# Optimization experiments

Measured on AMD Instinct MI355X. Metric: run time of the kernel, lower is better.

The kernel has to match this reference:

```python
import jax, jax.numpy as jnp
import numpy as np

B, T, C = 16, 512, 768
MULT = 4
D_IN = C * MULT          # 3072
HIDDEN = 1024
N_DATES = 16
STACK_SIZE, STACK_STRIDE = 4, 2
MAX_F = 512
N_MASK_TYPES = 5
N_SESSIONS = 4
SCALE = HIDDEN ** 0.5


def setup_inputs() -> dict:
    key = jax.random.key(0)
    ks = jax.random.split(key, 12)
    inp = {
        "spikes": jax.random.normal(ks[0], (B, T, C), dtype=jnp.float32),
        "spikes_mask": jnp.ones((B, T), dtype=jnp.int64),
        "spikes_timestamp": jax.random.randint(ks[1], (B, T), 0, 255).astype(jnp.int64),
        "date_idx": jax.random.randint(ks[2], (B,), 0, N_DATES).astype(jnp.int64),
        "mask_idx": 1,
        "session_idx": 3,
        # params
        "W_embed": jax.random.normal(ks[3], (N_DATES, D_IN, C), dtype=jnp.float32) * 0.02,
        "b_embed": jax.random.normal(ks[4], (N_DATES, D_IN), dtype=jnp.float32) * 0.02,
        "W_stack": jax.random.normal(ks[5], (HIDDEN, D_IN * STACK_SIZE), dtype=jnp.float32) * 0.02,
        "b_stack": jax.random.normal(ks[6], (HIDDEN,), dtype=jnp.float32) * 0.02,
        "pos_table": jax.random.normal(ks[7], (MAX_F, HIDDEN), dtype=jnp.float32) * 0.02,
        "prompt_table": jax.random.normal(ks[8], (N_MASK_TYPES, HIDDEN), dtype=jnp.float32) * 0.02,
        "session_table": jax.random.normal(ks[9], (N_SESSIONS, HIDDEN), dtype=jnp.float32) * 0.02,
    }
    return inp


def reference(spikes, spikes_mask, spikes_timestamp, date_idx, mask_idx, session_idx,
              W_embed, b_embed, W_stack, b_stack, pos_table, prompt_table, session_table):
    Bb = spikes.shape[0]
    # adapt branch: per-sample expert Linear, done as one gather + batched GEMM
    W = W_embed[date_idx]                      # [B, D_IN, C]
    b = b_embed[date_idx]                      # [B, D_IN]
    x = jnp.einsum('btc,bdc->btd', spikes, W) + b[:, None, :]   # [B, T, D_IN]
    x = jax.nn.gelu(x, approximate=False) * SCALE
    # unfold-based stacking: sliding windows over time
    L = (T - STACK_SIZE) // STACK_STRIDE + 1   # 255
    starts = jnp.arange(L) * STACK_STRIDE
    widx = starts[:, None] + jnp.arange(STACK_SIZE)             # [L, size]
    win = x[:, widx, :]                                         # [B, L, size, D_IN]
    stacked = win.reshape(Bb, L, STACK_SIZE * D_IN)
    x = stacked @ W_stack.T + b_stack                           # [B, L, HIDDEN]
    ts = spikes_timestamp[:, :L]
    mask = jnp.prod(spikes_mask[:, widx], axis=-1)              # [B, L]
    # positional embedding
    x = x + pos_table[ts]
    # prompt token
    x = jnp.concatenate(
        [jnp.broadcast_to(prompt_table[mask_idx][None, None, :], (Bb, 1, HIDDEN)), x], axis=1)
    mask = jnp.pad(mask, ((0, 0), (1, 0)), constant_values=1)
    ts = jnp.concatenate([jnp.zeros((Bb, 1), ts.dtype), ts + 1], axis=1)
    # session token
    x = jnp.concatenate(
        [jnp.broadcast_to(session_table[session_idx][None, None, :], (Bb, 1, HIDDEN)), x], axis=1)
    mask = jnp.pad(mask, ((0, 0), (1, 0)), constant_values=1)
    ts = jnp.concatenate([jnp.zeros((Bb, 1), ts.dtype), ts + 1], axis=1)
    # dropout is identity in eval
    return x, mask, ts
```

## Files before the change

kernel.cpp:

```cpp
#include <hip/hip_runtime.h>
#include <hip/hip_bf16.h>

#define BATCH   16
#define TT      512
#define CC      768
#define D_IN    3072
#define HIDDEN  1024
#define LL      255
#define OUTROWS 257
#define KSTACK  12288
#define N_DATES 16

typedef float f32x4 __attribute__((ext_vector_type(4)));
typedef __bf16 bf16x8 __attribute__((ext_vector_type(8)));
typedef unsigned short u16;

__device__ __forceinline__ u16 f2bf(float f) {
    unsigned u = __builtin_bit_cast(unsigned, f);
    u = (u + 0x7FFFu + ((u >> 16) & 1u)) >> 16;
    return (u16)u;
}

__device__ __forceinline__ bf16x8 lds_read8(const u16* p) {
    return __builtin_bit_cast(bf16x8, *(const uint4*)p);
}

__device__ __forceinline__ void gload16(const u16* g, u16* l) {
    __builtin_amdgcn_global_load_lds(
        (const __attribute__((address_space(1))) void*)g,
        (__attribute__((address_space(3))) void*)l, 16, 0, 0);
}

__global__ __launch_bounds__(256) void cvt_wstack(const float* __restrict__ W, u16* __restrict__ out) {
    size_t i = ((size_t)blockIdx.x * 256 + threadIdx.x) * 4;
    size_t stride = (size_t)gridDim.x * 256 * 4;
    for (; i < (size_t)HIDDEN * KSTACK; i += stride) {
        float4 v = *(const float4*)(W + i);
        ushort4 o = make_ushort4(f2bf(v.x), f2bf(v.y), f2bf(v.z), f2bf(v.w));
        *(ushort4*)(out + i) = o;
    }
}

__global__ __launch_bounds__(256) void cvt_spikes(const float* __restrict__ in, u16* __restrict__ out) {
    size_t i = ((size_t)blockIdx.x * 256 + threadIdx.x) * 4;
    size_t stride = (size_t)gridDim.x * 256 * 4;
    for (; i < (size_t)BATCH * TT * CC; i += stride) {
        float4 v = *(const float4*)(in + i);
        ushort4 o = make_ushort4(f2bf(v.x), f2bf(v.y), f2bf(v.z), f2bf(v.w));
        *(ushort4*)(out + i) = o;
    }
}

__global__ __launch_bounds__(64) void date_flags(const int* __restrict__ date_idx, int* __restrict__ flags) {
    const int tid = threadIdx.x;
    if (tid < N_DATES) flags[tid] = 0;
    __syncthreads();
    if (tid < BATCH) flags[date_idx[tid]] = 1;
}

__global__ __launch_bounds__(256) void cvt_wembed(const float* __restrict__ W,
                                                  const int* __restrict__ flags,
                                                  u16* __restrict__ out) {
    const int date = blockIdx.y;
    if (!flags[date]) return;
    const size_t bofs = (size_t)date * D_IN * CC;
    const size_t i = bofs + ((size_t)blockIdx.x * 256 + threadIdx.x) * 4;
    float4 v = *(const float4*)(W + i);
    ushort4 o = make_ushort4(f2bf(v.x), f2bf(v.y), f2bf(v.z), f2bf(v.w));
    *(ushort4*)(out + i) = o;
}

__global__ __launch_bounds__(512, 2) void gemm1_bf(const u16* __restrict__ spk,
                                                   const u16* __restrict__ wemb,
                                                   const float* __restrict__ b_embed,
                                                   const int* __restrict__ date_idx,
                                                   u16* __restrict__ x1) {
    const int m0 = blockIdx.x * 256;
    const int n0 = blockIdx.y * 256;
    const int bb = blockIdx.z;
    const int date = date_idx[bb];
    const u16* A  = spk  + (size_t)bb   * TT * CC;
    const u16* Bw = wemb + (size_t)date * D_IN * CC;
    const int nt = CC / 64;

    __shared__ u16 Asm[2 * 256 * 64];
    __shared__ u16 Bsm[2 * 256 * 64];

    const int tid  = threadIdx.x;
    const int lane = tid & 63;
    const int wave = tid >> 6;
    const int wm = wave >> 2;
    const int wn = wave & 3;

    const int lrow = lane >> 3;
    const int scol = ((lane & 7) ^ lrow) << 3;

    f32x4 acc[8][4] = {};

    auto STAGE = [&](int k0, int buf) {
        u16* Ad = Asm + buf * (256 * 64);
        u16* Bd = Bsm + buf * (256 * 64);
        #pragma unroll
        for (int i = 0; i < 4; ++i) {
            const int rb = i * 8 + wave;
            const int row = rb * 8 + lrow;
            gload16(A  + (size_t)(m0 + row) * CC + k0 + scol, Ad + rb * 512);
            gload16(Bw + (size_t)(n0 + row) * CC + k0 + scol, Bd + rb * 512);
        }
    };

    STAGE(0, 0);
    STAGE(64, 1);

    for (int t = 0; t < nt; ++t) {
        const int cur = t & 1;
        if (t + 1 < nt) { asm volatile("s_waitcnt vmcnt(8)" ::: "memory"); }
        else            { asm volatile("s_waitcnt vmcnt(0)" ::: "memory"); }
        __builtin_amdgcn_s_barrier();
        asm volatile("" ::: "memory");

        const u16* Ab = Asm + cur * (256 * 64);
        const u16* Bb = Bsm + cur * (256 * 64);
        #pragma unroll
        for (int kk = 0; kk < 64; kk += 32) {
            bf16x8 af[8], bfr[4];
            const int krow = lane & 15;
            const int kcol = kk + ((lane >> 4) << 3);
            #pragma unroll
            for (int i = 0; i < 8; ++i) {
                const int ra = wm * 128 + i * 16 + krow;
                af[i] = lds_read8(&Ab[ra * 64 + (kcol ^ ((ra & 7) << 3))]);
            }
            #pragma unroll
            for (int j = 0; j < 4; ++j) {
                const int rb2 = wn * 64 + j * 16 + krow;
                bfr[j] = lds_read8(&Bb[rb2 * 64 + (kcol ^ ((rb2 & 7) << 3))]);
            }
            #pragma unroll
            for (int i = 0; i < 8; ++i)
                #pragma unroll
                for (int j = 0; j < 4; ++j)
                    acc[i][j] = __builtin_amdgcn_mfma_f32_16x16x32_bf16(af[i], bfr[j], acc[i][j], 0, 0, 0);
        }

        asm volatile("" ::: "memory");
        __builtin_amdgcn_s_barrier();
        asm volatile("" ::: "memory");
        if (t + 2 < nt) STAGE((t + 2) * 64, cur);
    }

    const float* be = b_embed + (size_t)date * D_IN;
    #pragma unroll
    for (int i = 0; i < 8; ++i) {
        #pragma unroll
        for (int j = 0; j < 4; ++j) {
            const int col  = n0 + wn * 64 + j * 16 + (lane & 15);
            const float bias = be[col];
            const int rbase = m0 + wm * 128 + i * 16 + ((lane >> 4) << 2);
            #pragma unroll
            for (int q = 0; q < 4; ++q) {
                float v = acc[i][j][q] + bias;
                float g = 0.5f * v * (1.0f + erff(v * 0.70710678118654752f)) * 32.0f;
                x1[(size_t)bb * TT * D_IN + (size_t)(rbase + q) * D_IN + col] = f2bf(g);
            }
        }
    }
}

__global__ __launch_bounds__(256) void gemm1_f32(const float* __restrict__ spikes,
                                                 const float* __restrict__ W_embed,
                                                 const float* __restrict__ b_embed,
                                                 const int* __restrict__ date_idx,
                                                 u16* __restrict__ x1) {
    const int m0 = blockIdx.x * 128;
    const int n0 = blockIdx.y * 128;
    const int bb = blockIdx.z;
    const int date = date_idx[bb];
    const float* A  = spikes  + (size_t)bb  * TT * CC;
    const float* Bw = W_embed + (size_t)date * D_IN * CC;

    __shared__ u16 As[128 * 64];
    __shared__ u16 Bs[128 * 64];

    const int tid  = threadIdx.x;
    const int lane = tid & 63;
    const int wave = tid >> 6;
    const int wm = wave >> 1, wn = wave & 1;

    f32x4 acc[4][4] = {};

    for (int k0 = 0; k0 < CC; k0 += 64) {
        {
            const int c4 = tid & 15;
            int r = tid >> 4;
            #pragma unroll
            for (int p = 0; p < 8; ++p, r += 16) {
                float4 va = *(const float4*)(A  + (size_t)(m0 + r) * CC + k0 + c4 * 4);
                float4 vb = *(const float4*)(Bw + (size_t)(n0 + r) * CC + k0 + c4 * 4);
                const int col = c4 * 4;
                const int idx = r * 64 + (col ^ ((r & 7) << 3));
                *(ushort4*)(&As[idx]) = make_ushort4(f2bf(va.x), f2bf(va.y), f2bf(va.z), f2bf(va.w));
                *(ushort4*)(&Bs[idx]) = make_ushort4(f2bf(vb.x), f2bf(vb.y), f2bf(vb.z), f2bf(vb.w));
            }
        }
        __syncthreads();
        #pragma unroll
        for (int kk = 0; kk < 64; kk += 32) {
            bf16x8 af[4], bfr[4];
            const int krow = lane & 15;
            const int kcol = kk + ((lane >> 4) << 3);
            #pragma unroll
            for (int i = 0; i < 4; ++i) {
                const int ra = wm * 64 + i * 16 + krow;
                af[i]  = lds_read8(&As[ra * 64 + (kcol ^ ((ra & 7) << 3))]);
                const int rb = wn * 64 + i * 16 + krow;
                bfr[i] = lds_read8(&Bs[rb * 64 + (kcol ^ ((rb & 7) << 3))]);
            }
            #pragma unroll
            for (int i = 0; i < 4; ++i)
                #pragma unroll
                for (int j = 0; j < 4; ++j)
                    acc[i][j] = __builtin_amdgcn_mfma_f32_16x16x32_bf16(af[i], bfr[j], acc[i][j], 0, 0, 0);
        }
        __syncthreads();
    }

    const float* be = b_embed + (size_t)date * D_IN;
    #pragma unroll
    for (int i = 0; i < 4; ++i) {
        #pragma unroll
        for (int j = 0; j < 4; ++j) {
            const int col  = n0 + wn * 64 + j * 16 + (lane & 15);
            const float bias = be[col];
            const int rbase = m0 + wm * 64 + i * 16 + ((lane >> 4) << 2);
            #pragma unroll
            for (int q = 0; q < 4; ++q) {
                float v = acc[i][j][q] + bias;
                float g = 0.5f * v * (1.0f + erff(v * 0.70710678118654752f)) * 32.0f;
                x1[(size_t)bb * TT * D_IN + (size_t)(rbase + q) * D_IN + col] = f2bf(g);
            }
        }
    }
}

template <bool WRITE_PART>
__global__ __launch_bounds__(512, 2) void gemm2(const u16* __restrict__ x1,
                                                const u16* __restrict__ Wbf,
                                                float* __restrict__ part,
                                                const float* __restrict__ b_stack,
                                                const float* __restrict__ pos_table,
                                                const int* __restrict__ tstamp,
                                                float* __restrict__ out,
                                                int KS) {
    const int n0 = blockIdx.x * 256;
    const int ks = blockIdx.y;
    const int bb = blockIdx.z;
    const int KCH  = KSTACK / KS;
    const int kbeg = ks * KCH;
    const int nt   = KCH / 64;
    const u16* Xb = x1 + (size_t)bb * TT * D_IN;

    __shared__ u16 Asm[2 * 256 * 64];
    __shared__ u16 Bsm[2 * 256 * 64];

    const int tid  = threadIdx.x;
    const int lane = tid & 63;
    const int wave = tid >> 6;
    const int wm = wave >> 2;
    const int wn = wave & 3;

    const int lrow = lane >> 3;
    const int scol = ((lane & 7) ^ lrow) << 3;

    f32x4 acc[8][4] = {};

    auto STAGE = [&](int k0, int buf) {
        const int s  = k0 / D_IN;
        const int d0 = k0 % D_IN;
        u16* Ad = Asm + buf * (256 * 64);
        u16* Bd = Bsm + buf * (256 * 64);
        #pragma unroll
        for (int i = 0; i < 4; ++i) {
            const int rb = i * 8 + wave;
            const int row = rb * 8 + lrow;
            int gl = row; if (gl > LL - 1) gl = LL - 1;
            gload16(Xb + (size_t)(2 * gl + s) * D_IN + d0 + scol, Ad + rb * 512);
            gload16(Wbf + (size_t)(n0 + row) * KSTACK + k0 + scol, Bd + rb * 512);
        }
    };

    STAGE(kbeg, 0);
    STAGE(kbeg + 64, 1);

    for (int t = 0; t < nt; ++t) {
        const int cur = t & 1;
        if (t + 1 < nt) { asm volatile("s_waitcnt vmcnt(8)" ::: "memory"); }
        else            { asm volatile("s_waitcnt vmcnt(0)" ::: "memory"); }
        __builtin_amdgcn_s_barrier();
        asm volatile("" ::: "memory");

        const u16* Ab = Asm + cur * (256 * 64);
        const u16* Bb = Bsm + cur * (256 * 64);
        #pragma unroll
        for (int kk = 0; kk < 64; kk += 32) {
            bf16x8 af[8], bfr[4];
            const int krow = lane & 15;
            const int kcol = kk + ((lane >> 4) << 3);
            #pragma unroll
            for (int i = 0; i < 8; ++i) {
                const int ra = wm * 128 + i * 16 + krow;
                af[i] = lds_read8(&Ab[ra * 64 + (kcol ^ ((ra & 7) << 3))]);
            }
            #pragma unroll
            for (int j = 0; j < 4; ++j) {
                const int rb2 = wn * 64 + j * 16 + krow;
                bfr[j] = lds_read8(&Bb[rb2 * 64 + (kcol ^ ((rb2 & 7) << 3))]);
            }
            #pragma unroll
            for (int i = 0; i < 8; ++i)
                #pragma unroll
                for (int j = 0; j < 4; ++j)
                    acc[i][j] = __builtin_amdgcn_mfma_f32_16x16x32_bf16(af[i], bfr[j], acc[i][j], 0, 0, 0);
        }

        asm volatile("" ::: "memory");
        __builtin_amdgcn_s_barrier();
        asm volatile("" ::: "memory");
        if (t + 2 < nt) STAGE(kbeg + (t + 2) * 64, cur);
    }

    if (WRITE_PART) {
        float* pt = part + ((size_t)(ks * BATCH + bb) * 256) * HIDDEN;
        #pragma unroll
        for (int i = 0; i < 8; ++i) {
            #pragma unroll
            for (int j = 0; j < 4; ++j) {
                const int col = n0 + wn * 64 + j * 16 + (lane & 15);
                const int rb  = wm * 128 + i * 16 + ((lane >> 4) << 2);
                #pragma unroll
                for (int q = 0; q < 4; ++q)
                    pt[(size_t)(rb + q) * HIDDEN + col] = acc[i][j][q];
            }
        }
    } else {
        #pragma unroll
        for (int i = 0; i < 8; ++i) {
            #pragma unroll
            for (int j = 0; j < 4; ++j) {
                const int col = n0 + wn * 64 + j * 16 + (lane & 15);
                const int lb  = wm * 128 + i * 16 + ((lane >> 4) << 2);
                #pragma unroll
                for (int q = 0; q < 4; ++q) {
                    const int l = lb + q;
                    if (l < LL) {
                        const int tsv = tstamp[bb * TT + l];
                        float v = acc[i][j][q] + b_stack[col] + pos_table[(size_t)tsv * HIDDEN + col];
                        out[(size_t)bb * OUTROWS * HIDDEN + (size_t)(2 + l) * HIDDEN + col] = v;
                    }
                }
            }
        }
    }
}

__global__ __launch_bounds__(256) void reduce_ep(const float* __restrict__ part,
                                                 const float* __restrict__ b_stack,
                                                 const float* __restrict__ pos_table,
                                                 const int* __restrict__ tstamp,
                                                 float* __restrict__ out,
                                                 int KS) {
    const int idx = blockIdx.x * 256 + threadIdx.x;
    const int c4  = idx & (HIDDEN / 4 - 1);
    const int r   = idx >> 8;
    if (r >= BATCH * LL) return;
    const int l  = r % LL;
    const int bb = r / LL;
    float4 v = make_float4(0.f, 0.f, 0.f, 0.f);
    for (int ks = 0; ks < KS; ++ks) {
        float4 p = *(const float4*)(part + ((size_t)(ks * BATCH + bb) * 256 + l) * HIDDEN + c4 * 4);
        v.x += p.x; v.y += p.y; v.z += p.z; v.w += p.w;
    }
    const int tsv = tstamp[bb * TT + l];
    float4 bs = *(const float4*)(b_stack + c4 * 4);
    float4 ps = *(const float4*)(pos_table + (size_t)tsv * HIDDEN + c4 * 4);
    v.x += bs.x + ps.x; v.y += bs.y + ps.y; v.z += bs.z + ps.z; v.w += bs.w + ps.w;
    *(float4*)(out + ((size_t)bb * OUTROWS + 2 + l) * HIDDEN + c4 * 4) = v;
}

__global__ __launch_bounds__(256) void epilogue_misc(const int* __restrict__ smask,
                                                     const int* __restrict__ tstamp,
                                                     const int* __restrict__ mask_idx_p,
                                                     const int* __restrict__ session_idx_p,
                                                     const float* __restrict__ prompt_table,
                                                     const float* __restrict__ session_table,
                                                     float* __restrict__ out) {
    const int bb = blockIdx.x;
    const int tid = threadIdx.x;
    const int mi = mask_idx_p[0];
    const int si = session_idx_p[0];
    float* xb = out + (size_t)bb * OUTROWS * HIDDEN;
    for (int i = tid; i < HIDDEN; i += 256) {
        xb[i]          = session_table[(size_t)si * HIDDEN + i];
        xb[HIDDEN + i] = prompt_table[(size_t)mi * HIDDEN + i];
    }
    float* maskout = out + (size_t)BATCH * OUTROWS * HIDDEN + (size_t)bb * OUTROWS;
    float* tsout   = out + (size_t)BATCH * OUTROWS * HIDDEN + (size_t)BATCH * OUTROWS + (size_t)bb * OUTROWS;
    for (int j = tid; j < OUTROWS; j += 256) {
        if (j == 0)      { maskout[0] = 1.0f; tsout[0] = 0.0f; }
        else if (j == 1) { maskout[1] = 1.0f; tsout[1] = 1.0f; }
        else {
            const int l = j - 2;
            int m = 1;
            #pragma unroll
            for (int s = 0; s < 4; ++s) m *= smask[bb * TT + 2 * l + s];
            maskout[j] = (float)m;
            tsout[j]   = (float)(tstamp[bb * TT + l] + 2);
        }
    }
}

extern "C" void kernel_launch(void* const* d_in, const int* in_sizes, int n_in,
                              void* d_out, int out_size, void* d_ws, size_t ws_size,
                              hipStream_t stream) {
    const float* spikes      = (const float*)d_in[0];
    const int*   spikes_mask = (const int*)d_in[1];
    const int*   tstamp      = (const int*)d_in[2];
    const int*   date_idx    = (const int*)d_in[3];
    const int*   mask_idx    = (const int*)d_in[4];
    const int*   session_idx = (const int*)d_in[5];
    const float* W_embed     = (const float*)d_in[6];
    const float* b_embed     = (const float*)d_in[7];
    const float* W_stack     = (const float*)d_in[8];
    const float* b_stack     = (const float*)d_in[9];
    const float* pos_table   = (const float*)d_in[10];
    const float* prompt_tab  = (const float*)d_in[11];
    const float* session_tab = (const float*)d_in[12];
    float* out = (float*)d_out;

    const size_t X1_B   = (size_t)BATCH * TT * D_IN * 2;
    const size_t WBF_B  = (size_t)HIDDEN * KSTACK * 2;
    const size_t PART_B = (size_t)BATCH * 256 * HIDDEN * 4;
    const size_t FLAGS_B = 4096;
    const size_t SPK_B  = (size_t)BATCH * TT * CC * 2;
    const size_t WEMB_B = (size_t)N_DATES * D_IN * CC * 2;
    const size_t BASE   = X1_B + WBF_B;
    const size_t UNION_BF = FLAGS_B + SPK_B + WEMB_B;

    u16*   x1    = (u16*)d_ws;
    u16*   Wbf   = (u16*)((char*)d_ws + X1_B);
    int*   flags = (int*)((char*)d_ws + BASE);
    u16*   spkbf = (u16*)((char*)d_ws + BASE + FLAGS_B);
    u16*   wembf = (u16*)((char*)d_ws + BASE + FLAGS_B + SPK_B);
    float* part  = (float*)((char*)d_ws + BASE);

    const bool use_bf = (ws_size >= BASE + UNION_BF);
    int KS = 0;
    if (use_bf) KS = 4;
    else {
        size_t rem = (ws_size > BASE) ? (ws_size - BASE) : 0;
        KS = (int)(rem / PART_B); if (KS > 4) KS = 4;
    }

    cvt_wstack<<<2048, 256, 0, stream>>>(W_stack, Wbf);

    if (use_bf) {
        date_flags<<<1, 64, 0, stream>>>(date_idx, flags);
        cvt_spikes<<<2048, 256, 0, stream>>>(spikes, spkbf);
        cvt_wembed<<<dim3(D_IN * CC / 4 / 256, N_DATES), 256, 0, stream>>>(W_embed, flags, wembf);
        gemm1_bf<<<dim3(TT / 256, D_IN / 256, BATCH), 512, 0, stream>>>(spkbf, wembf, b_embed, date_idx, x1);
    } else {
        gemm1_f32<<<dim3(TT / 128, D_IN / 128, BATCH), 256, 0, stream>>>(spikes, W_embed, b_embed, date_idx, x1);
    }

    if (KS > 0) {
        gemm2<true><<<dim3(HIDDEN / 256, KS, BATCH), 512, 0, stream>>>(x1, Wbf, part, b_stack, pos_table, tstamp, out, KS);
        reduce_ep<<<(BATCH * LL * (HIDDEN / 4) + 255) / 256, 256, 0, stream>>>(part, b_stack, pos_table, tstamp, out, KS);
    } else {
        gemm2<false><<<dim3(HIDDEN / 256, 1, BATCH), 512, 0, stream>>>(x1, Wbf, part, b_stack, pos_table, tstamp, out, 1);
    }
    epilogue_misc<<<BATCH, 256, 0, stream>>>(spikes_mask, tstamp, mask_idx, session_idx,
                                             prompt_tab, session_tab, out);
}
```

Baseline: 265.0 us.

## Use 4-slot 32-wide K pipeline with one barrier per step in gemm2

Restructures the stacking GEMM's main loop from a double-buffered 64-wide K tile with two barriers per iteration into a 4-slot ring of 32-wide K slices, three slices in flight, and a single barrier per step. The LDS layout packs two rows' half-tiles per 64-element line. The next slice is issued right after fragments are read, and the MFMA block is wrapped in s_setprio to favour math issue. This aims to hide global-load latency and cut barrier stalls, at the cost of more complex swizzle indexing and finer-grained waitcnt bookkeeping that must match the load count.

```diff
diff --git a/kernel.cpp b/kernel.cpp
--- a/kernel.cpp
+++ b/kernel.cpp
@@ -257,11 +257,11 @@
     const int bb = blockIdx.z;
     const int KCH  = KSTACK / KS;
     const int kbeg = ks * KCH;
-    const int nt   = KCH / 64;
+    const int S    = KCH / 32;
     const u16* Xb = x1 + (size_t)bb * TT * D_IN;
 
-    __shared__ u16 Asm[2 * 256 * 64];
-    __shared__ u16 Bsm[2 * 256 * 64];
+    __shared__ u16 Asm[4][128 * 64];
+    __shared__ u16 Bsm[4][128 * 64];
 
     const int tid  = threadIdx.x;
     const int lane = tid & 63;
@@ -269,64 +269,64 @@
     const int wm = wave >> 2;
     const int wn = wave & 3;
 
-    const int lrow = lane >> 3;
-    const int scol = ((lane & 7) ^ lrow) << 3;
+    const int lrow  = lane >> 3;
+    const int scol  = ((lane & 7) ^ lrow) << 3;
+    const int chalf = scol >> 5;
+    const int gk    = scol & 31;
 
     f32x4 acc[8][4] = {};
 
-    auto STAGE = [&](int k0, int buf) {
+    auto STAGE = [&](int slice) {
+        const int slot = slice & 3;
+        const int k0 = kbeg + slice * 32;
         const int s  = k0 / D_IN;
         const int d0 = k0 % D_IN;
-        u16* Ad = Asm + buf * (256 * 64);
-        u16* Bd = Bsm + buf * (256 * 64);
-        #pragma unroll
-        for (int i = 0; i < 4; ++i) {
-            const int rb = i * 8 + wave;
-            const int row = rb * 8 + lrow;
-            int gl = row; if (gl > LL - 1) gl = LL - 1;
-            gload16(Xb + (size_t)(2 * gl + s) * D_IN + d0 + scol, Ad + rb * 512);
-            gload16(Wbf + (size_t)(n0 + row) * KSTACK + k0 + scol, Bd + rb * 512);
+        u16* Ad = Asm[slot];
+        u16* Bd = Bsm[slot];
+        #pragma unroll
+        for (int p = 0; p < 2; ++p) {
+            const int rbase = (wave + 8 * p) * 8;
+            const int u  = rbase + lrow;
+            const int tr = 2 * u + chalf;
+            int gl = tr; if (gl > LL - 1) gl = LL - 1;
+            gload16(Xb + (size_t)(2 * gl + s) * D_IN + d0 + gk, Ad + rbase * 64);
+            gload16(Wbf + (size_t)(n0 + tr) * KSTACK + k0 + gk, Bd + rbase * 64);
         }
     };
 
-    STAGE(kbeg, 0);
-    STAGE(kbeg + 64, 1);
-
-    for (int t = 0; t < nt; ++t) {
-        const int cur = t & 1;
-        if (t + 1 < nt) { asm volatile("s_waitcnt vmcnt(8)" ::: "memory"); }
-        else            { asm volatile("s_waitcnt vmcnt(0)" ::: "memory"); }
+    STAGE(0); STAGE(1); STAGE(2);
+
+    const int krow  = lane & 15;
+    const int kcol  = (lane >> 4) << 3;
+    const int cfrag = (kcol + ((krow & 1) << 5)) ^ ((krow >> 1) << 3);
+    const int urow  = krow >> 1;
+
+    for (int ph = 0; ph < S; ++ph) {
+        if (ph < S - 2)       { asm volatile("s_waitcnt vmcnt(8)" ::: "memory"); }
+        else if (ph == S - 2) { asm volatile("s_waitcnt vmcnt(4)" ::: "memory"); }
+        else                  { asm volatile("s_waitcnt vmcnt(0)" ::: "memory"); }
         __builtin_amdgcn_s_barrier();
         asm volatile("" ::: "memory");
 
-        const u16* Ab = Asm + cur * (256 * 64);
-        const u16* Bb = Bsm + cur * (256 * 64);
-        #pragma unroll
-        for (int kk = 0; kk < 64; kk += 32) {
-            bf16x8 af[8], bfr[4];
-            const int krow = lane & 15;
-            const int kcol = kk + ((lane >> 4) << 3);
-            #pragma unroll
-            for (int i = 0; i < 8; ++i) {
-                const int ra = wm * 128 + i * 16 + krow;
-                af[i] = lds_read8(&Ab[ra * 64 + (kcol ^ ((ra & 7) << 3))]);
-            }
-            #pragma unroll
-            for (int j = 0; j < 4; ++j) {
-                const int rb2 = wn * 64 + j * 16 + krow;
-                bfr[j] = lds_read8(&Bb[rb2 * 64 + (kcol ^ ((rb2 & 7) << 3))]);
-            }
-            #pragma unroll
-            for (int i = 0; i < 8; ++i)
-                #pragma unroll
-                for (int j = 0; j < 4; ++j)
-                    acc[i][j] = __builtin_amdgcn_mfma_f32_16x16x32_bf16(af[i], bfr[j], acc[i][j], 0, 0, 0);
-        }
-
-        asm volatile("" ::: "memory");
-        __builtin_amdgcn_s_barrier();
-        asm volatile("" ::: "memory");
-        if (t + 2 < nt) STAGE(kbeg + (t + 2) * 64, cur);
+        const u16* Ab = Asm[ph & 3];
+        const u16* Bb = Bsm[ph & 3];
+        bf16x8 af[8], bfr[4];
+        #pragma unroll
+        for (int i = 0; i < 8; ++i)
+            af[i] = lds_read8(&Ab[(wm * 64 + i * 8 + urow) * 64 + cfrag]);
+        #pragma unroll
+        for (int j = 0; j < 4; ++j)
+            bfr[j] = lds_read8(&Bb[(wn * 32 + j * 8 + urow) * 64 + cfrag]);
+
+        if (ph + 3 < S) STAGE(ph + 3);
+
+        __builtin_amdgcn_s_setprio(1);
+        #pragma unroll
+        for (int i = 0; i < 8; ++i)
+            #pragma unroll
+            for (int j = 0; j < 4; ++j)
+                acc[i][j] = __builtin_amdgcn_mfma_f32_16x16x32_bf16(af[i], bfr[j], acc[i][j], 0, 0, 0);
+        __builtin_amdgcn_s_setprio(0);
     }
 
     if (WRITE_PART) {
```

New measurement: 246.1 us. 1.08x faster.
